# Kernel tuning notes

Measured on AMD Instinct MI355X. Metric: run time of the kernel, lower is better.

The kernel has to match this reference:

```python
import jax, jax.numpy as jnp
import numpy as np

NQ = 10          # qubits
NT = 32          # tokens (LCU terms)
DM = 512         # d_model
DEG = 2          # qsvt degree
B = 128          # batch
NPQC = 4 * NQ    # params per PQC application
DIM = 2 ** NQ    # statevector dimension


def ansatz14_spec(q, layers=1):
    spec = []
    for _ in range(layers):
        spec += [('ry', (i,)) for i in range(q)]
        spec += [('crx', (i, (i + 1) % q)) for i in range(q - 1, -1, -1)]
        spec += [('ry', (i,)) for i in range(q)]
        spec += [('crx', (i, (i - 1) % q)) for i in [q - 1] + list(range(q - 1))]
    return spec

SPEC = ansatz14_spec(NQ, 1)


def _gate_ry(theta):
    h = theta * 0.5
    c = jnp.cos(h)
    s = jnp.sin(h)
    m = jnp.stack([jnp.stack([c, -s], -1), jnp.stack([s, c], -1)], -2)
    return m.astype(jnp.complex64)  # (N,2,2)


def _gate_rx(theta):
    h = theta * 0.5
    c = jnp.cos(h).astype(jnp.complex64)
    s = (-1j) * jnp.sin(h).astype(jnp.complex64)
    return jnp.stack([jnp.stack([c, s], -1), jnp.stack([s, c], -1)], -2)


def _apply_1q(state, mats, wire, q):
    # state: (N, 2^q) complex; mats: (N,2,2); wire 0 is most significant bit
    N = state.shape[0]
    a = 2 ** wire
    bdim = 2 ** (q - wire - 1)
    s = state.reshape(N, a, 2, bdim)
    return jnp.einsum('nij,najb->naib', mats, s).reshape(N, 2 ** q)


def _apply_crx(state, theta, c, t, q):
    # controlled-RX: control wire c, target wire t
    N = state.shape[0]
    st = state.reshape((N,) + (2,) * q)
    ax = 1 + c
    s0 = jnp.take(st, 0, axis=ax)   # control = 0 branch: untouched
    s1 = jnp.take(st, 1, axis=ax)   # control = 1 branch: apply RX on target
    tp = t if t < c else t - 1      # target wire position after removing control axis
    s1n = _apply_1q(s1.reshape(N, -1), _gate_rx(theta), tp, q - 1).reshape(s1.shape)
    return jnp.stack([s0, s1n], axis=ax).reshape(N, 2 ** q)


def _apply_pqc(state, params, q):
    # params: (N, NPQC); fixed small gate list -> Python loop is fine
    for k, (fn, w) in enumerate(SPEC):
        th = params[:, k]
        if fn == 'ry':
            state = _apply_1q(state, _gate_ry(th), w[0], q)
        else:
            state = _apply_crx(state, th, w[0], w[1], q)
    return state


def _apply_lcu(states, params, lcu):
    # states: (B, DIM) complex; params: (B, L, NPQC); lcu: (B, L) complex
    Bn, L = lcu.shape
    rep = jnp.repeat(states, L, axis=0)                    # (B*L, DIM)
    st = _apply_pqc(rep, params.reshape(Bn * L, NPQC), NQ)
    return jnp.einsum('bld,bl->bd', st.reshape(Bn, L, DIM), lcu)


def _measure_xyz(state, q):
    # Pauli expectations per wire: order [X_0..X_{q-1}, Y_0.., Z_0..]
    N = state.shape[0]
    xs, ys, zs = [], [], []
    for w in range(q):
        s = state.reshape(N, 2 ** w, 2, -1)
        a0, a1 = s[:, :, 0, :], s[:, :, 1, :]
        cross = jnp.sum(jnp.conj(a0) * a1, axis=(1, 2))
        xs.append(2.0 * jnp.real(cross))
        ys.append(2.0 * jnp.imag(cross))
        zs.append(jnp.sum(jnp.abs(a0) ** 2 - jnp.abs(a1) ** 2, axis=(1, 2)))
    return jnp.stack(xs + ys + zs, axis=1).astype(jnp.float32)  # (B, 3q)


def reference(tokens_emb, W, b, lcu_re, lcu_im, qsvt_coeffs, ff_params):
    Bn, L, D = tokens_emb.shape
    L = min(L, NT)
    pqc_params = tokens_emb[:, :L] @ W.T + b               # (B, L, NPQC)
    lcu = (lcu_re + 1j * lcu_im).astype(jnp.complex64)[:L]
    lcu = lcu / jnp.sum(jnp.abs(lcu))
    lcu_b = jnp.broadcast_to(lcu[None], (Bn, L))
    init = jnp.zeros((Bn, DIM), jnp.complex64).at[:, 0].set(1.0)
    acc = qsvt_coeffs[0].astype(jnp.complex64) * init
    mono = init
    for k in range(1, DEG + 1):
        mono = _apply_lcu(mono, pqc_params, lcu_b)
        acc = acc + qsvt_coeffs[k].astype(jnp.complex64) * mono
    state = acc / jnp.sum(jnp.abs(qsvt_coeffs))
    state = state / jnp.linalg.norm(state, axis=-1, keepdims=True)
    ffp = jnp.broadcast_to(ff_params[None], (Bn, NPQC))
    state = _apply_pqc(state, ffp, NQ)
    return _measure_xyz(state, NQ)


def setup_inputs():
    key = jax.random.key(0)
    ks = jax.random.split(key, 7)
    return {
        'tokens_emb': jax.random.normal(ks[0], (B, NT, DM), jnp.float32),
        'W': jax.random.normal(ks[1], (NPQC, DM), jnp.float32) * 0.05,
        'b': jax.random.normal(ks[2], (NPQC,), jnp.float32),
        'lcu_re': jax.random.normal(ks[3], (NT,), jnp.float32),
        'lcu_im': jax.random.normal(ks[4], (NT,), jnp.float32),
        'qsvt_coeffs': jax.random.normal(ks[5], (DEG + 1,), jnp.float32),
        'ff_params': jax.random.normal(ks[6], (NPQC,), jnp.float32),
    }
```

## Files before the change

### kernel.cpp

```cpp
#include <hip/hip_runtime.h>
#include <hip/hip_bf16.h>


#define NQ   10
#define NT   32
#define DM   512
#define BATCH 128
#define NPQC 40
#define DIM  1024
#define NROWS (BATCH * NT)
#define PSTRIDE (BATCH * DIM)

typedef float v2f __attribute__((ext_vector_type(2)));

#define WAITLDS asm volatile("s_waitcnt lgkmcnt(0)" ::: "memory")

__device__ __forceinline__ v2f Jrot(v2f v) {
  return __builtin_shufflevector(v, -v, 1, 2);
}
__device__ __forceinline__ v2f Jc(v2f v) {
  return __builtin_shufflevector(-v, v, 1, 2);
}


template<int B>
__device__ __forceinline__ void g_ry(v2f (&a)[16], float c, float s) {
  static_assert(B >= 6, "RY targets must be register bits");
  constexpr int m = 1 << (B - 6);
#pragma unroll
  for (int r = 0; r < 16; ++r) {
    if (!(r & m)) {
      int r1 = r | m;
      v2f a0 = a[r], a1 = a[r1];
      a[r]  = c * a0 - s * a1;
      a[r1] = s * a0 + c * a1;
    }
  }
}

template<int BC, int BT>
__device__ __forceinline__ void g_crx(v2f (&a)[16], int lane, float c, float s) {
  static_assert(BT >= 6, "CRX targets must be register bits");
  constexpr int m = 1 << (BT - 6);
  bool lane_ok = (BC >= 6) || ((lane >> BC) & 1);
  float ce = lane_ok ? c : 1.f;
  float se = lane_ok ? s : 0.f;
#pragma unroll
  for (int r = 0; r < 16; ++r) {
    if (!(r & m)) {
      if constexpr (BC >= 6) { if (!((r >> (BC - 6)) & 1)) continue; }
      int r1 = r | m;
      v2f a0 = a[r], a1 = a[r1];
      a[r]  = ce * a0 + se * Jrot(a1);
      a[r1] = ce * a1 + se * Jrot(a0);
    }
  }
}

template<int L0, int L1, int L2, int L3>
__device__ __forceinline__ void remap(v2f (&a)[16], v2f* __restrict__ slab,
                                      int lane) {
  constexpr int LM = (1 << L0) | (1 << L1) | (1 << L2) | (1 << L3);
#pragma unroll
  for (int r = 0; r < 16; ++r) {
    int f = 0;
    if (L0 < 4 && (r & 1)) f |= 1 << L0;
    if (L1 < 4 && (r & 2)) f |= 1 << L1;
    if (L2 < 4 && (r & 4)) f |= 1 << L2;
    if (L3 < 4 && (r & 8)) f |= 1 << L3;
    slab[r * 64 + (lane ^ f)] = a[r];
  }
  WAITLDS;
  int la = lane & ~LM & 63;
  la |= ((lane >> L0) & 1) << 6;
  la |= ((lane >> L1) & 1) << 7;
  la |= ((lane >> L2) & 1) << 8;
  la |= ((lane >> L3) & 1) << 9;
  if (L0 < 4) la |= ((lane >> L0) & 1) << L0;
  if (L1 < 4) la |= ((lane >> L1) & 1) << L1;
  if (L2 < 4) la |= ((lane >> L2) & 1) << L2;
  if (L3 < 4) la |= ((lane >> L3) & 1) << L3;
#pragma unroll
  for (int r = 0; r < 16; ++r) {
    int rc = ((r & 1) ? (1 << L0) : 0) | ((r & 2) ? (1 << L1) : 0)
           | ((r & 4) ? (1 << L2) : 0) | ((r & 8) ? (1 << L3) : 0);
    a[r] = slab[la ^ rc];
  }
}

template<bool SKIP_HEAD>
__device__ __forceinline__ void apply_pqc_phased(v2f (&a)[16],
    const float2* __restrict__ cs, v2f* __restrict__ slab, int lane) {
#define RYt(B, t)      g_ry<B>(a, t.x, t.y);
#define CXt(BC, BT, t) g_crx<BC, BT>(a, lane, t.x, t.y);
  float2 t10 = cs[10], t11 = cs[11], t12 = cs[12];
  if constexpr (!SKIP_HEAD) {
    float2 t0 = cs[0], t1 = cs[1], t2 = cs[2], t3 = cs[3];
    float2 t4 = cs[4], t5 = cs[5], t6 = cs[6], t7 = cs[7];
    float2 t8 = cs[8], t9 = cs[9];
    RYt(9,t0) RYt(8,t1) RYt(7,t2) RYt(6,t3)
    remap<5,4,3,2>(a, slab, lane);
    RYt(6,t4) RYt(7,t5) RYt(8,t6) RYt(9,t7)
    remap<1,0,2,3>(a, slab, lane);
    RYt(6,t8) RYt(7,t9)
  }
  CXt(7,8,t10) CXt(6,7,t11) CXt(3,6,t12)
  float2 t13 = cs[13], t14 = cs[14], t15 = cs[15], t16 = cs[16];
  remap<1,0,2,3>(a, slab, lane);
  CXt(8,9,t13) CXt(7,8,t14) CXt(6,7,t15) CXt(5,6,t16)
  float2 t17 = cs[17], t18 = cs[18], t19 = cs[19];
  float2 t20 = cs[20], t21 = cs[21], t22 = cs[22], t23 = cs[23];
  remap<2,3,4,5>(a, slab, lane);
  CXt(8,9,t17) CXt(7,8,t18) CXt(6,7,t19)
  RYt(6,t20) RYt(7,t21) RYt(8,t22) RYt(9,t23)
  float2 t24 = cs[24], t25 = cs[25], t26 = cs[26], t27 = cs[27];
  remap<2,3,4,5>(a, slab, lane);
  RYt(6,t24) RYt(7,t25) RYt(8,t26) RYt(9,t27)
  float2 t28 = cs[28], t29 = cs[29];
  float2 t30 = cs[30], t31 = cs[31], t32 = cs[32], t33 = cs[33];
  remap<1,0,2,3>(a, slab, lane);
  RYt(6,t28) RYt(7,t29)
  CXt(7,6,t30) CXt(8,7,t31) CXt(9,8,t32) CXt(4,9,t33)
  float2 t34 = cs[34], t35 = cs[35], t36 = cs[36], t37 = cs[37];
  remap<4,5,1,0>(a, slab, lane);
  CXt(7,6,t34) CXt(8,7,t35) CXt(9,8,t36) CXt(2,9,t37)
  float2 t38 = cs[38], t39 = cs[39];
  remap<2,3,4,5>(a, slab, lane);
  CXt(7,6,t38) CXt(8,7,t39)
#undef RYt
#undef CXt
}

__device__ __forceinline__ int p8_lane_canon(int lane) {
  return (((lane >> 1) & 1) << 9) | ((lane & 1) << 8) | (((lane >> 2) & 1) << 7)
       | (((lane >> 3) & 1) << 6) | (((lane >> 4) & 1) << 5) | (((lane >> 5) & 1) << 4);
}

__global__ __launch_bounds__(256) void params_kernel(
    const float* __restrict__ emb, const float* __restrict__ W,
    const float* __restrict__ bias,
    const float* __restrict__ lcu_re, const float* __restrict__ lcu_im,
    const float* __restrict__ ffp,
    float2* __restrict__ cs, float2* __restrict__ ffcs, float2* __restrict__ lcu) {
  int blk = blockIdx.x;
  int tid = threadIdx.x;
  if (blk == 256) {
    if (tid < NPQC) {
      float h = 0.5f * ffp[tid];
      ffcs[tid] = make_float2(cosf(h), sinf(h));
    }
    if (tid == 64) {
      float ssum = 0.f;
      for (int i = 0; i < NT; ++i) {
        float re = lcu_re[i], im = lcu_im[i];
        ssum += sqrtf(re * re + im * im);
      }
      float inv = 1.f / ssum;
      for (int i = 0; i < NT; ++i)
        lcu[i] = make_float2(lcu_re[i] * inv, lcu_im[i] * inv);
    }
    return;
  }

  __shared__ float Asl[16 * 516];
  int row0 = blk * 16;

  const float4* eg = (const float4*)(emb + (size_t)row0 * DM);
#pragma unroll
  for (int i = 0; i < 8; ++i) {
    int e = tid + i * 256;
    int r = e >> 7, k4 = e & 127;
    float4 v = eg[e];
    *(float4*)&Asl[r * 516 + k4 * 4] = v;
  }
  __syncthreads();

  int kq = tid >> 6;
  int lane = tid & 63;
  int rg = lane >> 3;
  int cg = lane & 7;

  const float* Ar0 = &Asl[(2 * rg) * 516 + kq * 128];
  const float* Ar1 = Ar0 + 516;
  const float* Bg  = W + (size_t)(5 * cg) * DM + kq * 128;

  float acc[2][5] = {};
#pragma unroll 4
  for (int k = 0; k < 128; k += 4) {
    float4 a0 = *(const float4*)(Ar0 + k);
    float4 a1 = *(const float4*)(Ar1 + k);
#pragma unroll
    for (int j = 0; j < 5; ++j) {
      float4 b = *(const float4*)(Bg + j * DM + k);
      acc[0][j] += a0.x * b.x + a0.y * b.y + a0.z * b.z + a0.w * b.w;
      acc[1][j] += a1.x * b.x + a1.y * b.y + a1.z * b.z + a1.w * b.w;
    }
  }

  __syncthreads();
  float* red = Asl;
#pragma unroll
  for (int i = 0; i < 2; ++i)
#pragma unroll
    for (int j = 0; j < 5; ++j)
      red[kq * 644 + (2 * rg + i) * 40 + 5 * cg + j] = acc[i][j];
  __syncthreads();

  for (int o = tid; o < 640; o += 256) {
    float v = bias[o % 40] + red[o] + red[644 + o] + red[1288 + o] + red[1932 + o];
    float h = 0.5f * v;
    cs[(size_t)blk * 640 + o] = make_float2(cosf(h), sinf(h));
  }
}

template<bool FIRST>
__global__ __launch_bounds__(256) void pqc_step(
    const float2* __restrict__ cs, const float2* __restrict__ lcu,
    const v2f* __restrict__ src, v2f* __restrict__ dst) {
  __shared__ v2f slabs[4][1024];
  int lane = threadIdx.x & 63;
  int wvu = __builtin_amdgcn_readfirstlane(threadIdx.x >> 6);
  int blk = blockIdx.x;
  int b = blk >> 3, qq = blk & 7;
  int l = qq * 4 + wvu;
  const float2* csrow = cs + (size_t)(b * NT + l) * NPQC;
  v2f* slab = slabs[wvu];

  v2f a[16];
  if constexpr (FIRST) {
    float2 f5 = csrow[5], f4 = csrow[4], f6 = csrow[6], f7 = csrow[7];
    float2 f2 = csrow[2], f3 = csrow[3];
    float2 f8 = csrow[8], f9 = csrow[9], f0 = csrow[0], f1 = csrow[1];
    float lp = ((lane & 1) ? f5.y : f5.x);
    lp *= ((lane & 2) ? f4.y : f4.x);
    lp *= ((lane & 4) ? f6.y : f6.x);
    lp *= ((lane & 8) ? f7.y : f7.x);
    lp *= ((lane & 16) ? f2.y : f2.x);
    lp *= ((lane & 32) ? f3.y : f3.x);
#pragma unroll
    for (int r = 0; r < 16; ++r) {
      float rp = ((r & 1) ? f8.y : f8.x) * ((r & 2) ? f9.y : f9.x)
               * ((r & 4) ? f0.y : f0.x) * ((r & 8) ? f1.y : f1.x);
      a[r].x = lp * rp;
      a[r].y = 0.f;
    }
  } else {
    const v2f* s = src + (size_t)b * DIM;
#pragma unroll
    for (int r = 0; r < 16; ++r) a[r] = s[r * 64 + lane];
  }

  apply_pqc_phased<FIRST>(a, csrow, slab, lane);

  float2 w = lcu[l];
  int pl = p8_lane_canon(lane);
  pl ^= (pl >> 5);
#pragma unroll
  for (int r = 0; r < 16; ++r) {
    int rc = ((r & 1) << 3) | ((r & 2) << 1) | ((r & 4) >> 1) | ((r & 8) >> 3);
    slab[pl ^ rc] = w.x * a[r] + w.y * Jc(a[r]);
  }
  __syncthreads();

  v2f* dst_b = dst + (size_t)(qq * BATCH + b) * DIM;
#pragma unroll
  for (int i = 0; i < 4; ++i) {
    int n = threadIdx.x + i * 256;
    int ph = n ^ (n >> 5);
    v2f sum = slabs[0][ph] + slabs[1][ph] + slabs[2][ph] + slabs[3][ph];
    dst_b[n] = sum;
  }
}


__global__ __launch_bounds__(256) void reduce_slices(v2f* __restrict__ buf) {
  int n = blockIdx.x * 256 + threadIdx.x;
  v2f acc = buf[n];
#pragma unroll
  for (int q = 1; q < 8; ++q) acc += buf[n + q * PSTRIDE];
  buf[n] = acc;
}

__global__ __launch_bounds__(256) void final_fused(
    const v2f* __restrict__ red1, const v2f* __restrict__ part2,
    const float* __restrict__ qsvt, const float2* __restrict__ ffcs,
    float* __restrict__ out) {
  __shared__ v2f st[1024];
  __shared__ float2 ang[40];
  __shared__ float rbuf[4];
  __shared__ float tb[30 * 257];
  int b = blockIdx.x, tid = threadIdx.x;
  int lane = tid & 63, wv = tid >> 6;
  float q0 = qsvt[0], q1 = qsvt[1], q2 = qsvt[2];
  const v2f* r1 = red1 + (size_t)b * DIM;
  const v2f* p2 = part2 + (size_t)b * DIM;

  if (tid < NPQC) ang[tid] = ffcs[tid];

  v2f vals[4];
  float nn = 0.f;
#pragma unroll
  for (int i = 0; i < 4; ++i) {
    int n = tid + i * 256;
    v2f m2 = p2[n];
#pragma unroll
    for (int q = 1; q < 8; ++q) m2 += p2[n + q * PSTRIDE];
    v2f v = q1 * r1[n] + q2 * m2;
    if (n == 0) v.x += q0;
    vals[i] = v;
    nn += v.x * v.x + v.y * v.y;
  }
#pragma unroll
  for (int o = 1; o < 64; o <<= 1) nn += __shfl_xor(nn, o);
  if (lane == 0) rbuf[wv] = nn;
  __syncthreads();
  float inv = 1.f / sqrtf(rbuf[0] + rbuf[1] + rbuf[2] + rbuf[3]);
#pragma unroll
  for (int i = 0; i < 4; ++i) {
    int n = tid + i * 256;
    st[n ^ (n >> 5)] = vals[i] * inv;
  }
  __syncthreads();

#pragma unroll 1
  for (int k = 0; k < NPQC; ++k) {
    int isCrx, c, t;
    if (k < 10)      { isCrx = 0; t = k;      c = 0; }
    else if (k < 20) { int i = 19 - k; isCrx = 1; c = i; t = (i == 9) ? 0 : i + 1; }
    else if (k < 30) { isCrx = 0; t = k - 20; c = 0; }
    else             { int i = (k == 30) ? 9 : k - 31; isCrx = 1; c = i; t = (i == 0) ? 9 : i - 1; }
    int m  = 1 << (9 - t);
    int cb = 9 - c;
    float2 th = ang[k];
    float cg = th.x, sg = th.y;

    v2f a0[2], a1[2];
    int j0[2], j1[2], en[2];
#pragma unroll
    for (int p = 0; p < 2; ++p) {
      int q  = p * 256 + tid;
      int i0 = ((q & ~(m - 1)) << 1) | (q & (m - 1));
      int i1 = i0 | m;
      j0[p] = i0 ^ (i0 >> 5);
      j1[p] = i1 ^ (i1 >> 5);
      en[p] = (i0 >> cb) & 1;
      a0[p] = st[j0[p]];
      a1[p] = st[j1[p]];
    }
#pragma unroll
    for (int p = 0; p < 2; ++p) {
      v2f n0, n1;
      if (!isCrx) {
        n0 = cg * a0[p] - sg * a1[p];
        n1 = sg * a0[p] + cg * a1[p];
      } else {
        float ce = en[p] ? cg : 1.f;
        float se = en[p] ? sg : 0.f;
        n0 = ce * a0[p] + se * Jrot(a1[p]);
        n1 = ce * a1[p] + se * Jrot(a0[p]);
      }
      st[j0[p]] = n0;
      st[j1[p]] = n1;
    }
    __syncthreads();
  }

#pragma unroll 1
  for (int w = 0; w < NQ; ++w) {
    int m = 1 << (9 - w);
    float xr = 0.f, xi = 0.f, zz = 0.f;
#pragma unroll
    for (int p = 0; p < 2; ++p) {
      int q  = p * 256 + tid;
      int i0 = ((q & ~(m - 1)) << 1) | (q & (m - 1));
      int i1 = i0 | m;
      v2f a0 = st[i0 ^ (i0 >> 5)];
      v2f a1 = st[i1 ^ (i1 >> 5)];
      xr += a0.x * a1.x + a0.y * a1.y;
      xi += a0.x * a1.y - a0.y * a1.x;
      zz += a0.x * a0.x + a0.y * a0.y - a1.x * a1.x - a1.y * a1.y;
    }
    tb[w * 257 + tid]        = xr;
    tb[(10 + w) * 257 + tid] = xi;
    tb[(20 + w) * 257 + tid] = zz;
  }
  __syncthreads();
  if (tid < 30) {
    float s2 = 0.f;
#pragma unroll 8
    for (int t = 0; t < 256; ++t) s2 += tb[tid * 257 + t];
    float sc = (tid < 20) ? 2.f : 1.f;
    out[b * 30 + tid] = sc * s2;
  }
}


extern "C" void kernel_launch(void* const* d_in, const int* in_sizes, int n_in,
                              void* d_out, int out_size, void* d_ws, size_t ws_size,
                              hipStream_t stream) {
  const float* emb    = (const float*)d_in[0];
  const float* W      = (const float*)d_in[1];
  const float* bias   = (const float*)d_in[2];
  const float* lcu_re = (const float*)d_in[3];
  const float* lcu_im = (const float*)d_in[4];
  const float* qsvt   = (const float*)d_in[5];
  const float* ffp    = (const float*)d_in[6];
  float* out = (float*)d_out;

  char* ws = (char*)d_ws;
  float2* cs    = (float2*)ws;
  float2* ffcs  = (float2*)(ws + 1310720);
  float2* lcu   = (float2*)(ws + 1311040);
  v2f*    part1 = (v2f*)(ws + 1311744);
  v2f*    part2 = (v2f*)(ws + 1311744 + 8388608);

  params_kernel<<<257, 256, 0, stream>>>(emb, W, bias, lcu_re, lcu_im, ffp,
                                         cs, ffcs, lcu);
  pqc_step<true><<<1024, 256, 0, stream>>>(cs, lcu, nullptr, part1);
  reduce_slices<<<512, 256, 0, stream>>>(part1);
  pqc_step<false><<<1024, 256, 0, stream>>>(cs, lcu, part1, part2);
  final_fused<<<BATCH, 256, 0, stream>>>(part1, part2, qsvt, ffcs, out);
}
```

Baseline: 151.3 us.

## Replace register-resident PQC with generic LDS gate loop per wave

Drops the hand-scheduled register statevector path, which used compile-time bit remaps between register and lane bits. Each wave now keeps its 1024-amplitude state in its LDS slab and applies all gates in a runtime loop over a gate descriptor, reading and writing pairs from shared memory. The LCU weighting moves out of the per-wave store and into the cross-wave reduction. This simplifies the code but makes every gate two LDS round trips instead of register arithmetic, so LDS traffic per gate rises sharply.

```diff
diff --git a/kernel.cpp b/kernel.cpp
--- a/kernel.cpp
+++ b/kernel.cpp
@@ -8,7 +8,6 @@
 #define BATCH 128
 #define NPQC 40
 #define DIM  1024
-#define NROWS (BATCH * NT)
 #define PSTRIDE (BATCH * DIM)
 
 typedef float v2f __attribute__((ext_vector_type(2)));
@@ -22,118 +21,14 @@
   return __builtin_shufflevector(-v, v, 1, 2);
 }
 
-
-template<int B>
-__device__ __forceinline__ void g_ry(v2f (&a)[16], float c, float s) {
-  static_assert(B >= 6, "RY targets must be register bits");
-  constexpr int m = 1 << (B - 6);
-#pragma unroll
-  for (int r = 0; r < 16; ++r) {
-    if (!(r & m)) {
-      int r1 = r | m;
-      v2f a0 = a[r], a1 = a[r1];
-      a[r]  = c * a0 - s * a1;
-      a[r1] = s * a0 + c * a1;
-    }
-  }
-}
-
-template<int BC, int BT>
-__device__ __forceinline__ void g_crx(v2f (&a)[16], int lane, float c, float s) {
-  static_assert(BT >= 6, "CRX targets must be register bits");
-  constexpr int m = 1 << (BT - 6);
-  bool lane_ok = (BC >= 6) || ((lane >> BC) & 1);
-  float ce = lane_ok ? c : 1.f;
-  float se = lane_ok ? s : 0.f;
-#pragma unroll
-  for (int r = 0; r < 16; ++r) {
-    if (!(r & m)) {
-      if constexpr (BC >= 6) { if (!((r >> (BC - 6)) & 1)) continue; }
-      int r1 = r | m;
-      v2f a0 = a[r], a1 = a[r1];
-      a[r]  = ce * a0 + se * Jrot(a1);
-      a[r1] = ce * a1 + se * Jrot(a0);
-    }
-  }
-}
-
-template<int L0, int L1, int L2, int L3>
-__device__ __forceinline__ void remap(v2f (&a)[16], v2f* __restrict__ slab,
-                                      int lane) {
-  constexpr int LM = (1 << L0) | (1 << L1) | (1 << L2) | (1 << L3);
-#pragma unroll
-  for (int r = 0; r < 16; ++r) {
-    int f = 0;
-    if (L0 < 4 && (r & 1)) f |= 1 << L0;
-    if (L1 < 4 && (r & 2)) f |= 1 << L1;
-    if (L2 < 4 && (r & 4)) f |= 1 << L2;
-    if (L3 < 4 && (r & 8)) f |= 1 << L3;
-    slab[r * 64 + (lane ^ f)] = a[r];
-  }
-  WAITLDS;
-  int la = lane & ~LM & 63;
-  la |= ((lane >> L0) & 1) << 6;
-  la |= ((lane >> L1) & 1) << 7;
-  la |= ((lane >> L2) & 1) << 8;
-  la |= ((lane >> L3) & 1) << 9;
-  if (L0 < 4) la |= ((lane >> L0) & 1) << L0;
-  if (L1 < 4) la |= ((lane >> L1) & 1) << L1;
-  if (L2 < 4) la |= ((lane >> L2) & 1) << L2;
-  if (L3 < 4) la |= ((lane >> L3) & 1) << L3;
-#pragma unroll
-  for (int r = 0; r < 16; ++r) {
-    int rc = ((r & 1) ? (1 << L0) : 0) | ((r & 2) ? (1 << L1) : 0)
-           | ((r & 4) ? (1 << L2) : 0) | ((r & 8) ? (1 << L3) : 0);
-    a[r] = slab[la ^ rc];
-  }
-}
-
-template<bool SKIP_HEAD>
-__device__ __forceinline__ void apply_pqc_phased(v2f (&a)[16],
-    const float2* __restrict__ cs, v2f* __restrict__ slab, int lane) {
-#define RYt(B, t)      g_ry<B>(a, t.x, t.y);
-#define CXt(BC, BT, t) g_crx<BC, BT>(a, lane, t.x, t.y);
-  float2 t10 = cs[10], t11 = cs[11], t12 = cs[12];
-  if constexpr (!SKIP_HEAD) {
-    float2 t0 = cs[0], t1 = cs[1], t2 = cs[2], t3 = cs[3];
-    float2 t4 = cs[4], t5 = cs[5], t6 = cs[6], t7 = cs[7];
-    float2 t8 = cs[8], t9 = cs[9];
-    RYt(9,t0) RYt(8,t1) RYt(7,t2) RYt(6,t3)
-    remap<5,4,3,2>(a, slab, lane);
-    RYt(6,t4) RYt(7,t5) RYt(8,t6) RYt(9,t7)
-    remap<1,0,2,3>(a, slab, lane);
-    RYt(6,t8) RYt(7,t9)
-  }
-  CXt(7,8,t10) CXt(6,7,t11) CXt(3,6,t12)
-  float2 t13 = cs[13], t14 = cs[14], t15 = cs[15], t16 = cs[16];
-  remap<1,0,2,3>(a, slab, lane);
-  CXt(8,9,t13) CXt(7,8,t14) CXt(6,7,t15) CXt(5,6,t16)
-  float2 t17 = cs[17], t18 = cs[18], t19 = cs[19];
-  float2 t20 = cs[20], t21 = cs[21], t22 = cs[22], t23 = cs[23];
-  remap<2,3,4,5>(a, slab, lane);
-  CXt(8,9,t17) CXt(7,8,t18) CXt(6,7,t19)
-  RYt(6,t20) RYt(7,t21) RYt(8,t22) RYt(9,t23)
-  float2 t24 = cs[24], t25 = cs[25], t26 = cs[26], t27 = cs[27];
-  remap<2,3,4,5>(a, slab, lane);
-  RYt(6,t24) RYt(7,t25) RYt(8,t26) RYt(9,t27)
-  float2 t28 = cs[28], t29 = cs[29];
-  float2 t30 = cs[30], t31 = cs[31], t32 = cs[32], t33 = cs[33];
-  remap<1,0,2,3>(a, slab, lane);
-  RYt(6,t28) RYt(7,t29)
-  CXt(7,6,t30) CXt(8,7,t31) CXt(9,8,t32) CXt(4,9,t33)
-  float2 t34 = cs[34], t35 = cs[35], t36 = cs[36], t37 = cs[37];
-  remap<4,5,1,0>(a, slab, lane);
-  CXt(7,6,t34) CXt(8,7,t35) CXt(9,8,t36) CXt(2,9,t37)
-  float2 t38 = cs[38], t39 = cs[39];
-  remap<2,3,4,5>(a, slab, lane);
-  CXt(7,6,t38) CXt(8,7,t39)
-#undef RYt
-#undef CXt
-}
-
-__device__ __forceinline__ int p8_lane_canon(int lane) {
-  return (((lane >> 1) & 1) << 9) | ((lane & 1) << 8) | (((lane >> 2) & 1) << 7)
-       | (((lane >> 3) & 1) << 6) | (((lane >> 4) & 1) << 5) | (((lane >> 5) & 1) << 4);
+__device__ __forceinline__ void gate_desc(int k, int& isCrx, int& m, int& cb) {
+  int c, t;
+  if (k < 10)      { isCrx = 0; t = k;      c = 0; }
+  else if (k < 20) { int i = 19 - k; isCrx = 1; c = i; t = (i == 9) ? 0 : i + 1; }
+  else if (k < 30) { isCrx = 0; t = k - 20; c = 0; }
+  else             { int i = (k == 30) ? 9 : k - 31; isCrx = 1; c = i; t = (i == 0) ? 9 : i - 1; }
+  m  = 1 << (9 - t);
+  cb = 9 - c;
 }
 
 __global__ __launch_bounds__(256) void params_kernel(
@@ -224,50 +119,92 @@
   int b = blk >> 3, qq = blk & 7;
   int l = qq * 4 + wvu;
   const float2* csrow = cs + (size_t)(b * NT + l) * NPQC;
-  v2f* slab = slabs[wvu];
-
-  v2f a[16];
+  v2f* st = slabs[wvu];
+
   if constexpr (FIRST) {
-    float2 f5 = csrow[5], f4 = csrow[4], f6 = csrow[6], f7 = csrow[7];
-    float2 f2 = csrow[2], f3 = csrow[3];
-    float2 f8 = csrow[8], f9 = csrow[9], f0 = csrow[0], f1 = csrow[1];
-    float lp = ((lane & 1) ? f5.y : f5.x);
-    lp *= ((lane & 2) ? f4.y : f4.x);
-    lp *= ((lane & 4) ? f6.y : f6.x);
-    lp *= ((lane & 8) ? f7.y : f7.x);
-    lp *= ((lane & 16) ? f2.y : f2.x);
-    lp *= ((lane & 32) ? f3.y : f3.x);
+    float2 f9 = csrow[9], f8 = csrow[8], f7 = csrow[7], f6 = csrow[6];
+    float2 f5 = csrow[5], f4 = csrow[4], f3 = csrow[3], f2 = csrow[2];
+    float2 f1 = csrow[1], f0 = csrow[0];
+    float lp = ((lane & 1) ? f9.y : f9.x);
+    lp *= ((lane & 2)  ? f8.y : f8.x);
+    lp *= ((lane & 4)  ? f7.y : f7.x);
+    lp *= ((lane & 8)  ? f6.y : f6.x);
+    lp *= ((lane & 16) ? f5.y : f5.x);
+    lp *= ((lane & 32) ? f4.y : f4.x);
 #pragma unroll
     for (int r = 0; r < 16; ++r) {
-      float rp = ((r & 1) ? f8.y : f8.x) * ((r & 2) ? f9.y : f9.x)
-               * ((r & 4) ? f0.y : f0.x) * ((r & 8) ? f1.y : f1.x);
-      a[r].x = lp * rp;
-      a[r].y = 0.f;
+      float rp = ((r & 1) ? f3.y : f3.x) * ((r & 2) ? f2.y : f2.x)
+               * ((r & 4) ? f1.y : f1.x) * ((r & 8) ? f0.y : f0.x);
+      int n = r * 64 + lane;
+      v2f v; v.x = lp * rp; v.y = 0.f;
+      st[n ^ (n >> 5)] = v;
     }
   } else {
     const v2f* s = src + (size_t)b * DIM;
 #pragma unroll
-    for (int r = 0; r < 16; ++r) a[r] = s[r * 64 + lane];
-  }
-
-  apply_pqc_phased<FIRST>(a, csrow, slab, lane);
-
-  float2 w = lcu[l];
-  int pl = p8_lane_canon(lane);
-  pl ^= (pl >> 5);
-#pragma unroll
-  for (int r = 0; r < 16; ++r) {
-    int rc = ((r & 1) << 3) | ((r & 2) << 1) | ((r & 4) >> 1) | ((r & 8) >> 3);
-    slab[pl ^ rc] = w.x * a[r] + w.y * Jc(a[r]);
-  }
-  __syncthreads();
-
+    for (int r = 0; r < 16; ++r) {
+      int n = r * 64 + lane;
+      st[n ^ (n >> 5)] = s[n];
+    }
+  }
+  WAITLDS;
+
+  constexpr int k0 = FIRST ? 10 : 0;
+  float2 th = csrow[k0];
+#pragma unroll 1
+  for (int k = k0; k < NPQC; ++k) {
+    float2 thn = csrow[(k + 1 < NPQC) ? k + 1 : k0];
+    int isCrx, m, cb;
+    gate_desc(k, isCrx, m, cb);
+    float cg = th.x, sg = th.y;
+
+    v2f a0[8], a1[8];
+    int j0[8], j1[8], en[8];
+#pragma unroll
+    for (int p = 0; p < 8; ++p) {
+      int qp = p * 64 + lane;
+      int i0 = ((qp & ~(m - 1)) << 1) | (qp & (m - 1));
+      int i1 = i0 | m;
+      j0[p] = i0 ^ (i0 >> 5);
+      j1[p] = i1 ^ (i1 >> 5);
+      en[p] = (i0 >> cb) & 1;
+      a0[p] = st[j0[p]];
+      a1[p] = st[j1[p]];
+    }
+    WAITLDS;
+#pragma unroll
+    for (int p = 0; p < 8; ++p) {
+      v2f n0, n1;
+      if (!isCrx) {
+        n0 = cg * a0[p] - sg * a1[p];
+        n1 = sg * a0[p] + cg * a1[p];
+      } else {
+        float ce = en[p] ? cg : 1.f;
+        float se = en[p] ? sg : 0.f;
+        n0 = ce * a0[p] + se * Jrot(a1[p]);
+        n1 = ce * a1[p] + se * Jrot(a0[p]);
+      }
+      st[j0[p]] = n0;
+      st[j1[p]] = n1;
+    }
+    WAITLDS;
+    th = thn;
+  }
+
+  __syncthreads();
+  float2 lw0 = lcu[qq * 4 + 0], lw1 = lcu[qq * 4 + 1];
+  float2 lw2 = lcu[qq * 4 + 2], lw3 = lcu[qq * 4 + 3];
   v2f* dst_b = dst + (size_t)(qq * BATCH + b) * DIM;
 #pragma unroll
   for (int i = 0; i < 4; ++i) {
     int n = threadIdx.x + i * 256;
     int ph = n ^ (n >> 5);
-    v2f sum = slabs[0][ph] + slabs[1][ph] + slabs[2][ph] + slabs[3][ph];
+    v2f v0 = slabs[0][ph], v1 = slabs[1][ph];
+    v2f v2 = slabs[2][ph], v3 = slabs[3][ph];
+    v2f sum = lw0.x * v0 + lw0.y * Jc(v0)
+            + lw1.x * v1 + lw1.y * Jc(v1)
+            + lw2.x * v2 + lw2.y * Jc(v2)
+            + lw3.x * v3 + lw3.y * Jc(v3);
     dst_b[n] = sum;
   }
 }
@@ -324,13 +261,8 @@
 
 #pragma unroll 1
   for (int k = 0; k < NPQC; ++k) {
-    int isCrx, c, t;
-    if (k < 10)      { isCrx = 0; t = k;      c = 0; }
-    else if (k < 20) { int i = 19 - k; isCrx = 1; c = i; t = (i == 9) ? 0 : i + 1; }
-    else if (k < 30) { isCrx = 0; t = k - 20; c = 0; }
-    else             { int i = (k == 30) ? 9 : k - 31; isCrx = 1; c = i; t = (i == 0) ? 9 : i - 1; }
-    int m  = 1 << (9 - t);
-    int cb = 9 - c;
+    int isCrx, m, cb;
+    gate_desc(k, isCrx, m, cb);
     float2 th = ang[k];
     float cg = th.x, sg = th.y;
 
@@ -338,8 +270,8 @@
     int j0[2], j1[2], en[2];
 #pragma unroll
     for (int p = 0; p < 2; ++p) {
-      int q  = p * 256 + tid;
-      int i0 = ((q & ~(m - 1)) << 1) | (q & (m - 1));
+      int qp = p * 256 + tid;
+      int i0 = ((qp & ~(m - 1)) << 1) | (qp & (m - 1));
       int i1 = i0 | m;
       j0[p] = i0 ^ (i0 >> 5);
       j1[p] = i1 ^ (i1 >> 5);
@@ -371,8 +303,8 @@
     float xr = 0.f, xi = 0.f, zz = 0.f;
 #pragma unroll
     for (int p = 0; p < 2; ++p) {
-      int q  = p * 256 + tid;
-      int i0 = ((q & ~(m - 1)) << 1) | (q & (m - 1));
+      int qp = p * 256 + tid;
+      int i0 = ((qp & ~(m - 1)) << 1) | (qp & (m - 1));
       int i1 = i0 | m;
       v2f a0 = st[i0 ^ (i0 >> 5)];
       v2f a1 = st[i1 ^ (i1 >> 5)];
```

New measurement: 237.0 us. +56.6%, slower.
